# Optimization experiments

Hardware: AMD Instinct MI355X
Metric: run time of the kernel (lower is better)

## Reference

```python
import jax, jax.numpy as jnp
import numpy as np

WEIGHT = 1.0  # init arg `weight`; `threshold` is unused in forward
B, N, M, D = 4, 4096, 4096, 3


def setup_inputs() -> dict:
    key = jax.random.key(0)
    k1, k2 = jax.random.split(key)
    coord = jax.random.normal(k1, (B, N, D), dtype=jnp.float32)
    gt = jax.random.normal(k2, (B, M, D), dtype=jnp.float32)
    return {"coord": coord, "gt": gt}


def reference(coord, gt):
    # Faithful to torch: gt/coord are [B, pts, 3]; transpose(2,1) -> [B, 3, pts]
    g = jnp.transpose(gt, (0, 2, 1))     # [B, 3, M]
    c = jnp.transpose(coord, (0, 2, 1))  # [B, 3, N]
    # dis[b, m, n] = sum_d (g[b,d,m] - c[b,d,n])^2  -> [B, M, N]
    dis = jnp.sum((g[:, :, :, None] - c[:, :, None, :]) ** 2, axis=1)
    match_gt = jnp.min(dis, axis=-1)     # [B, M] nearest coord for each gt point
    match_coord = jnp.min(dis, axis=-2)  # [B, N] nearest gt point for each coord
    res = jnp.mean(match_coord) + jnp.mean(match_gt)
    return WEIGHT * res
```

## Files before the change

kernel.cpp:

```cpp
#include <hip/hip_runtime.h>


#define NPTS 4096
#define TILE 32
#define G    8

__global__ __launch_bounds__(256) void chamfer_pack(
    const float* __restrict__ coord, const float* __restrict__ gt,
    float4* __restrict__ packed)
{
    int i = blockIdx.x * 256 + threadIdx.x;
    const float* src = (i < 16384) ? (coord + i * 3)
                                   : (gt + (i - 16384) * 3);
    float x = src[0], y = src[1], z = src[2];
    packed[i] = make_float4(x, y, z, fmaf(x, x, fmaf(y, y, z * z)));
}

__global__ __launch_bounds__(256, 4) void chamfer_pass(
    const float4* __restrict__ packed, float* __restrict__ partials)
{
    const float4* pc = packed;
    const float4* pg = packed + 16384;

    int bx   = blockIdx.x;
    int pass = bx >> 9;
    int r    = bx & 511;
    int b    = r >> 7;
    int tile = r & 127;

    const float4* hb = (pass ? pc : pg) + b * NPTS;
    const float4* sb = (pass ? pg : pc) + b * NPTS;

    int tid = threadIdx.x;
    int hg  = tid >> 6;
    int ph  = tid & 63;

    float hx[G], hy[G], hz[G], h2[G], mn[G];
    int h0 = tile * TILE + hg * G;
#pragma unroll
    for (int g = 0; g < G; ++g) {
        float4 h = hb[h0 + g];
        hx[g] = -2.f * h.x;
        hy[g] = -2.f * h.y;
        hz[g] = -2.f * h.z;
        h2[g] = h.w;
        mn[g] = INFINITY;
    }

    const float4* s = sb + ph;
#pragma unroll 8
    for (int it = 0; it < 32; ++it) {
        float4 c0 = s[it * 128];
        float4 c1 = s[it * 128 + 64];
#pragma unroll
        for (int g = 0; g < G; ++g) {
            float a = fmaf(c0.x, hx[g], c0.w);
            a = fmaf(c0.y, hy[g], a);
            a = fmaf(c0.z, hz[g], a);
            float d = fmaf(c1.x, hx[g], c1.w);
            d = fmaf(c1.y, hy[g], d);
            d = fmaf(c1.z, hz[g], d);
            mn[g] = fminf(fminf(a, d), mn[g]);
        }
    }

    __shared__ float bsum[4];
    float ssum = 0.f;
#pragma unroll
    for (int g = 0; g < G; ++g) {
        float v = mn[g];
        v = fminf(v, __shfl_xor(v, 32));
        v = fminf(v, __shfl_xor(v, 16));
        v = fminf(v, __shfl_xor(v, 8));
        v = fminf(v, __shfl_xor(v, 4));
        v = fminf(v, __shfl_xor(v, 2));
        v = fminf(v, __shfl_xor(v, 1));
        ssum += fmaxf(v + h2[g], 0.f);
    }
    if (ph == 0) bsum[hg] = ssum;
    __syncthreads();
    if (tid == 0)
        partials[bx] = bsum[0] + bsum[1] + bsum[2] + bsum[3];
}

__global__ __launch_bounds__(256) void chamfer_final(
    const float* __restrict__ partials, float* __restrict__ out)
{
    __shared__ float wsum[4];
    int tid = threadIdx.x;
    float s = 0.f;
#pragma unroll
    for (int k = 0; k < 4; ++k)
        s += partials[k * 256 + tid];
#pragma unroll
    for (int off = 32; off > 0; off >>= 1)
        s += __shfl_down(s, off);
    if ((tid & 63) == 0) wsum[tid >> 6] = s;
    __syncthreads();
    if (tid == 0)
        out[0] = (wsum[0] + wsum[1] + wsum[2] + wsum[3]) * (1.0f / 16384.0f);
}

extern "C" void kernel_launch(void* const* d_in, const int* in_sizes, int n_in,
                              void* d_out, int out_size, void* d_ws, size_t ws_size,
                              hipStream_t stream) {
    const float* coord = (const float*)d_in[0];
    const float* gt    = (const float*)d_in[1];
    float4* packed   = (float4*)d_ws;
    float*  partials = (float*)((char*)d_ws + 32768 * sizeof(float4));
    float*  out      = (float*)d_out;

    chamfer_pack<<<128, 256, 0, stream>>>(coord, gt, packed);
    chamfer_pass<<<1024, 256, 0, stream>>>(packed, partials);
    chamfer_final<<<1, 256, 0, stream>>>(partials, out);
}
```

Measured before the change: 72.60 us.

## Stage search points in LDS and double block size to 512 threads

```diff
diff --git a/kernel.cpp b/kernel.cpp
--- a/kernel.cpp
+++ b/kernel.cpp
@@ -2,7 +2,7 @@
 
 
 #define NPTS 4096
-#define TILE 32
+#define TILE 64
 #define G    8
 
 __global__ __launch_bounds__(256) void chamfer_pack(
@@ -16,27 +16,33 @@
     packed[i] = make_float4(x, y, z, fmaf(x, x, fmaf(y, y, z * z)));
 }
 
-__global__ __launch_bounds__(256, 4) void chamfer_pass(
+__global__ __launch_bounds__(512, 4) void chamfer_pass(
     const float4* __restrict__ packed, float* __restrict__ partials)
 {
+    __shared__ float4 sc[NPTS];
+
     const float4* pc = packed;
     const float4* pg = packed + 16384;
 
     int bx   = blockIdx.x;
-    int pass = bx >> 9;
-    int r    = bx & 511;
-    int b    = r >> 7;
-    int tile = r & 127;
+    int pass = bx >> 8;
+    int r    = bx & 255;
+    int b    = r >> 6;
+    int tile = r & 63;
 
     const float4* hb = (pass ? pc : pg) + b * NPTS;
     const float4* sb = (pass ? pg : pc) + b * NPTS;
 
     int tid = threadIdx.x;
-    int hg  = tid >> 6;
+    int wv  = tid >> 6;
     int ph  = tid & 63;
 
+#pragma unroll
+    for (int rr = 0; rr < 8; ++rr)
+        sc[rr * 512 + tid] = sb[rr * 512 + tid];
+
     float hx[G], hy[G], hz[G], h2[G], mn[G];
-    int h0 = tile * TILE + hg * G;
+    int h0 = tile * TILE + wv * G;
 #pragma unroll
     for (int g = 0; g < G; ++g) {
         float4 h = hb[h0 + g];
@@ -46,12 +52,12 @@
         h2[g] = h.w;
         mn[g] = INFINITY;
     }
+    __syncthreads();
 
-    const float4* s = sb + ph;
 #pragma unroll 8
     for (int it = 0; it < 32; ++it) {
-        float4 c0 = s[it * 128];
-        float4 c1 = s[it * 128 + 64];
+        float4 c0 = sc[it * 128 + ph];
+        float4 c1 = sc[it * 128 + 64 + ph];
 #pragma unroll
         for (int g = 0; g < G; ++g) {
             float a = fmaf(c0.x, hx[g], c0.w);
@@ -64,7 +70,6 @@
         }
     }
 
-    __shared__ float bsum[4];
     float ssum = 0.f;
 #pragma unroll
     for (int g = 0; g < G; ++g) {
@@ -77,10 +82,17 @@
         v = fminf(v, __shfl_xor(v, 1));
         ssum += fmaxf(v + h2[g], 0.f);
     }
-    if (ph == 0) bsum[hg] = ssum;
+
     __syncthreads();
-    if (tid == 0)
-        partials[bx] = bsum[0] + bsum[1] + bsum[2] + bsum[3];
+    float* red = (float*)sc;
+    if (ph == 0) red[wv] = ssum;
+    __syncthreads();
+    if (tid == 0) {
+        float t = 0.f;
+#pragma unroll
+        for (int k = 0; k < 8; ++k) t += red[k];
+        partials[bx] = t;
+    }
 }
 
 __global__ __launch_bounds__(256) void chamfer_final(
@@ -88,10 +100,7 @@
 {
     __shared__ float wsum[4];
     int tid = threadIdx.x;
-    float s = 0.f;
-#pragma unroll
-    for (int k = 0; k < 4; ++k)
-        s += partials[k * 256 + tid];
+    float s = partials[tid] + partials[tid + 256];
 #pragma unroll
     for (int off = 32; off > 0; off >>= 1)
         s += __shfl_down(s, off);
@@ -111,6 +120,6 @@
     float*  out      = (float*)d_out;
 
     chamfer_pack<<<128, 256, 0, stream>>>(coord, gt, packed);
-    chamfer_pass<<<1024, 256, 0, stream>>>(packed, partials);
+    chamfer_pass<<<512, 512, 0, stream>>>(packed, partials);
     chamfer_final<<<1, 256, 0, stream>>>(partials, out);
 }
```

After: 72.56 us. About the same (-0.1%).
